# Kernel optimization log

Measured on AMD Instinct MI355X. Metric: run time of the kernel, lower is better.

## Reference

```python
import jax, jax.numpy as jnp
import numpy as np

NEG_SLOPE = 0.2

def _leaky(x):
    return jnp.where(x >= 0, x, NEG_SLOPE * x)

def _unigat(X, W, b, ae, av, pair_e, pair_v, num_v, num_e):
    # theta
    Xp = X @ W + b                                                    # [N, d]
    # v2e mean aggregation -> hyperedge features
    deg_e = jax.ops.segment_sum(jnp.ones(pair_e.shape, jnp.float32), pair_e, num_segments=num_e)
    Y = jax.ops.segment_sum(Xp[pair_v], pair_e, num_segments=num_e) / jnp.maximum(deg_e, 1.0)[:, None]  # [E, d]
    # GAT-style attention per incidence pair (edge term + node term), dropout=identity in eval
    s = _leaky((Y @ ae)[pair_e] + (Xp @ av)[pair_v])                  # [P]
    # segment softmax over edges incident to each node
    m = jax.ops.segment_max(s, pair_v, num_segments=num_v)
    ex = jnp.exp(s - m[pair_v])
    den = jax.ops.segment_sum(ex, pair_v, num_segments=num_v)
    alpha = ex / den[pair_v]                                          # [P]
    out = jax.ops.segment_sum(alpha[:, None] * Y[pair_e], pair_v, num_segments=num_v)  # [N, d]
    return jax.nn.elu(out)  # is_last=False everywhere -> ELU (use_bn=False)

def _multi_head(X, W, b, ae, av, pair_e, pair_v, num_v, num_e):
    # W:[H,din,d] b:[H,d] ae/av:[H,d]; concat heads on feature dim
    f = lambda Wh, bh, aeh, avh: _unigat(X, Wh, bh, aeh, avh, pair_e, pair_v, num_v, num_e)
    outs = jax.vmap(f)(W, b, ae, av)                                  # [H, N, d]
    return jnp.transpose(outs, (1, 0, 2)).reshape(X.shape[0], -1)     # [N, H*d]

def setup_inputs() -> dict:
    key = jax.random.key(0)
    ks = jax.random.split(key, 12)
    N, E, P = 100000, 20000, 1600000
    din, dh, H, C = 128, 64, 4, 40
    concat = 2
    inp = {
        "x0": jax.random.normal(ks[0], (N, din), jnp.float32),
        "x1": jax.random.normal(ks[1], (N, din), jnp.float32),
        "W1": jax.random.normal(ks[2], (H, din, dh), jnp.float32) * 0.05,
        "b1": jnp.zeros((H, dh), jnp.float32),
        "ae1": jax.random.normal(ks[3], (H, dh), jnp.float32) * 0.05,
        "av1": jax.random.normal(ks[4], (H, dh), jnp.float32) * 0.05,
        "W2": jax.random.normal(ks[5], (concat * dh * H, C), jnp.float32) * 0.05,
        "b2": jnp.zeros((C,), jnp.float32),
        "ae2": jax.random.normal(ks[6], (C,), jnp.float32) * 0.05,
        "av2": jax.random.normal(ks[7], (C,), jnp.float32) * 0.05,
        "pair_e": jax.random.randint(ks[8], (P,), 0, E, jnp.int32),
        "pair_v": jax.random.randint(ks[9], (P,), 0, N, jnp.int32),
        "num_v": N,
        "num_e": E,
    }
    return inp

def reference(x0, x1, W1, b1, ae1, av1, W2, b2, ae2, av2, pair_e, pair_v, num_v, num_e):
    # dropout layers are identity in eval mode
    h0 = _multi_head(x0, W1, b1, ae1, av1, pair_e, pair_v, num_v, num_e)
    h1 = _multi_head(x1, W1, b1, ae1, av1, pair_e, pair_v, num_v, num_e)
    h = jnp.concatenate([h0, h1], axis=-1)                            # [N, concat*H*dh]
    return _unigat(h, W2, b2, ae2, av2, pair_e, pair_v, num_v, num_e) # [N, C]
```

## Files before the change

### kernel.cpp

```cpp
#include <hip/hip_runtime.h>
#include <cstdint>
#include <cstddef>

static constexpr int DIN = 128;
static constexpr int DH = 64;
static constexpr int NH = 4;
static constexpr int DCAT = 512;
static constexpr int NC = 40;
static constexpr int E_CONST = 20000;
static constexpr int SH_V = 9, SUBD_V = 512;
static constexpr int SH_E = 7, SUBD_E = 128;
static constexpr int ECH = 11, NSUB_E = 10;
static constexpr int VCH = 12, NSUB_V = 25;
static constexpr int CHUNKA = 4096;

typedef unsigned short u16;
typedef __attribute__((ext_vector_type(4))) unsigned short u16x4;
typedef __attribute__((ext_vector_type(8))) unsigned short u16x8;
typedef __attribute__((ext_vector_type(8))) short bf16x8;
typedef __attribute__((ext_vector_type(4))) float f32x4;

static __device__ __forceinline__ float bf2f(u16 u) {
    union { unsigned int i; float f; } x;
    x.i = ((unsigned int)u) << 16;
    return x.f;
}
static __device__ __forceinline__ u16 f2bf(float f) {
    union { float f; unsigned int i; } x;
    x.f = f;
    unsigned int r = x.i + 0x7fffu + ((x.i >> 16) & 1u);
    return (u16)(r >> 16);
}


__global__ void k_hist2(const int* __restrict__ pv, const int* __restrict__ pe,
                        int* __restrict__ btot_v, int* __restrict__ btot_e, int P) {
    __shared__ int cv[256], ce[256];
    int tid = threadIdx.x;
    cv[tid] = 0; ce[tid] = 0;
    __syncthreads();
    int p0 = blockIdx.x * CHUNKA;
    #pragma unroll
    for (int j = 0; j < CHUNKA / 256; ++j) {
        int p = p0 + tid + j * 256;
        if (p < P) {
            atomicAdd(&cv[pv[p] >> SH_V], 1);
            atomicAdd(&ce[pe[p] >> SH_E], 1);
        }
    }
    __syncthreads();
    if (cv[tid]) atomicAdd(&btot_v[tid], cv[tid]);
    if (ce[tid]) atomicAdd(&btot_e[tid], ce[tid]);
}

__global__ void k_scan_small(int* __restrict__ a, int n) {
    __shared__ int wsum[16];
    __shared__ int carry_s;
    int tid = threadIdx.x;
    int lane = tid & 63;
    int w = tid >> 6;
    if (tid == 0) carry_s = 0;
    __syncthreads();
    for (int base = 0; base < n; base += 1024) {
        int i = base + tid;
        int v = (i < n) ? a[i] : 0;
        int x = v;
        #pragma unroll
        for (int off = 1; off < 64; off <<= 1) {
            int t = __shfl_up(x, off);
            if (lane >= off) x += t;
        }
        if (lane == 63) wsum[w] = x;
        __syncthreads();
        int woff = 0;
        for (int k = 0; k < w; ++k) woff += wsum[k];
        int carry = carry_s;
        if (i < n) a[i] = carry + woff + x - v;
        int tot = 0;
        for (int k = 0; k < 16; ++k) tot += wsum[k];
        __syncthreads();
        if (tid == 0) carry_s = carry + tot;
        __syncthreads();
    }
    if (tid == 0) a[n] = carry_s;
}

__global__ void k_scatter2way(const int* __restrict__ pv, const int* __restrict__ pe,
                              const int* __restrict__ bstart_v, const int* __restrict__ bstart_e,
                              int* __restrict__ cur_v, int* __restrict__ cur_e,
                              uint2* __restrict__ sorted_v, uint2* __restrict__ sorted_e, int P) {
    __shared__ int cv[256], ce[256], posv[256], pose[256];
    int tid = threadIdx.x;
    cv[tid] = 0; ce[tid] = 0;
    __syncthreads();
    int p0 = blockIdx.x * CHUNKA;
    int kv[CHUNKA / 256], ke[CHUNKA / 256];
    #pragma unroll
    for (int j = 0; j < CHUNKA / 256; ++j) {
        int p = p0 + tid + j * 256;
        if (p < P) {
            kv[j] = pv[p];
            ke[j] = pe[p];
            atomicAdd(&cv[kv[j] >> SH_V], 1);
            atomicAdd(&ce[ke[j] >> SH_E], 1);
        } else {
            kv[j] = -1;
            ke[j] = -1;
        }
    }
    __syncthreads();
    if (cv[tid]) posv[tid] = bstart_v[tid] + atomicAdd(&cur_v[tid], cv[tid]);
    if (ce[tid]) pose[tid] = bstart_e[tid] + atomicAdd(&cur_e[tid], ce[tid]);
    __syncthreads();
    #pragma unroll
    for (int j = 0; j < CHUNKA / 256; ++j) {
        if (kv[j] >= 0) {
            int iv = atomicAdd(&posv[kv[j] >> SH_V], 1);
            sorted_v[iv] = make_uint2((unsigned)kv[j], (unsigned)ke[j]);
            int ie = atomicAdd(&pose[ke[j] >> SH_E], 1);
            sorted_e[ie] = make_uint2((unsigned)ke[j], (unsigned)kv[j]);
        }
    }
}

template <int SUBD, int SH, int NSUB, int CSH>
__global__ __launch_bounds__(256) void k_build_ord(const uint2* __restrict__ sorted,
                                                   const int* __restrict__ bstart,
                                                   int* __restrict__ start_out,
                                                   int* __restrict__ deg_out,
                                                   int* __restrict__ csr_out, int D) {
    constexpr int NK2 = SUBD * NSUB;
    constexpr int STRIP = (NK2 + 255) / 256;
    __shared__ int cnt[NK2];
    __shared__ int wsum[4];
    int b = blockIdx.x;
    int tid = threadIdx.x;
    int base_key = b << SH;
    int s0 = bstart[b];
    int cntN = bstart[b + 1] - s0;
    for (int k = tid; k < NK2; k += 256) cnt[k] = 0;
    __syncthreads();
    for (int i = tid; i < cntN; i += 256) {
        uint2 pr = sorted[s0 + i];
        int k2 = ((int)pr.x - base_key) * NSUB + ((int)pr.y >> CSH);
        atomicAdd(&cnt[k2], 1);
    }
    __syncthreads();
    int local[STRIP];
    int sum = 0;
    int t0 = tid * STRIP;
    #pragma unroll
    for (int j = 0; j < STRIP; ++j) {
        int idx = t0 + j;
        local[j] = (idx < NK2) ? cnt[idx] : 0;
        sum += local[j];
    }
    int lane = tid & 63, w = tid >> 6;
    int x = sum;
    #pragma unroll
    for (int off = 1; off < 64; off <<= 1) {
        int t = __shfl_up(x, off);
        if (lane >= off) x += t;
    }
    if (lane == 63) wsum[w] = x;
    __syncthreads();
    int woff = 0;
    for (int k = 0; k < w; ++k) woff += wsum[k];
    int run = woff + x - sum;
    __syncthreads();
    #pragma unroll
    for (int j = 0; j < STRIP; ++j) {
        int idx = t0 + j;
        if (idx < NK2) {
            int tmp = local[j];
            cnt[idx] = run;
            run += tmp;
        }
    }
    __syncthreads();
    for (int loc = tid; loc < SUBD; loc += 256) {
        int key = base_key + loc;
        if (key < D) {
            int st = cnt[loc * NSUB];
            int en = (loc == SUBD - 1) ? cntN : cnt[(loc + 1) * NSUB];
            start_out[key] = s0 + st;
            deg_out[key] = en - st;
        }
    }
    __syncthreads();
    for (int i = tid; i < cntN; i += 256) {
        uint2 pr = sorted[s0 + i];
        int k2 = ((int)pr.x - base_key) * NSUB + ((int)pr.y >> CSH);
        int idx = atomicAdd(&cnt[k2], 1);
        csr_out[s0 + idx] = (int)pr.y;
    }
}


__global__ void k_wav(const float* __restrict__ W1, const float* __restrict__ b1,
                      const float* __restrict__ av1, float* __restrict__ wav,
                      float* __restrict__ bav) {
    int h = blockIdx.x;
    int k = threadIdx.x;
    float s = 0.f;
    for (int j = 0; j < DH; ++j) s += W1[(size_t)(h * DIN + k) * DH + j] * av1[h * DH + j];
    wav[h * DIN + k] = s;
    if (k == 0) {
        float t = 0.f;
        for (int j = 0; j < DH; ++j) t += b1[h * DH + j] * av1[h * DH + j];
        bav[h] = t;
    }
}

__global__ void k_build_wcatT(const float* __restrict__ W1, u16* __restrict__ WcatT) {
    int idx = blockIdx.x * 256 + threadIdx.x;
    if (idx >= 256 * DIN) return;
    int c = idx >> 7, k = idx & 127;
    int h = c >> 6, j = c & 63;
    WcatT[c * DIN + k] = f2bf(W1[((size_t)h * DIN + k) * DH + j]);
}

__global__ void k_build_w2T(const float* __restrict__ W2, u16* __restrict__ W2T) {
    int idx = blockIdx.x * 256 + threadIdx.x;
    if (idx >= 48 * DCAT) return;
    int c = idx >> 9, k = idx & 511;
    float v = (c < NC) ? W2[(size_t)k * NC + c] : 0.f;
    W2T[c * DCAT + k] = f2bf(v);
}

__global__ void k_conv(const float* __restrict__ X0, const float* __restrict__ X1,
                       const float* __restrict__ wav, const float* __restrict__ bav,
                       u16* __restrict__ Xbi, float* __restrict__ sv8, int N) {
    int wave = (blockIdx.x * blockDim.x + threadIdx.x) >> 6;
    int lane = threadIdx.x & 63;
    if (wave >= N) return;
    int xz = blockIdx.y;
    const float* X = xz ? X1 : X0;
    float2 a = *(const float2*)(X + (size_t)wave * DIN + lane * 2);
    unsigned int packed = (unsigned int)f2bf(a.x) | ((unsigned int)f2bf(a.y) << 16);
    *(unsigned int*)(Xbi + (size_t)wave * 256 + xz * 128 + lane * 2) = packed;
    float s[NH];
    #pragma unroll
    for (int h = 0; h < NH; ++h) {
        float2 wv = *(const float2*)(wav + h * DIN + lane * 2);
        float t = a.x * wv.x + a.y * wv.y;
        #pragma unroll
        for (int off = 32; off >= 1; off >>= 1) t += __shfl_xor(t, off);
        s[h] = t;
    }
    if (lane == 0) {
        #pragma unroll
        for (int h = 0; h < NH; ++h) sv8[(size_t)(xz * 4 + h) * N + wave] = s[h] + bav[h];
    }
}

__global__ void k_edge_mean1(const u16* __restrict__ Xbi, const int* __restrict__ start_e,
                             const int* __restrict__ deg_e, const int* __restrict__ csr_e_v,
                             u16* __restrict__ Xbar0, u16* __restrict__ Xbar1, int E) {
    int wave = (blockIdx.x * blockDim.x + threadIdx.x) >> 6;
    int lane = threadIdx.x & 63;
    if (wave >= E) return;
    int s = start_e[wave], t = s + deg_e[wave];
    int q = lane >> 4, c = lane & 15;
    float a0[8], a1[8];
    #pragma unroll
    for (int j = 0; j < 8; ++j) { a0[j] = 0.f; a1[j] = 0.f; }
    int i = s + q;
    u16x8 y0A = {0}, y1A = {0}, y0B = {0}, y1B = {0}, y0C = {0}, y1C = {0};
#define EM1_LOAD(Y0, Y1, IDX) { int v_ = csr_e_v[IDX]; \
        const u16* yp_ = Xbi + (size_t)v_ * 256 + c * 8; \
        Y0 = *(const u16x8*)yp_; Y1 = *(const u16x8*)(yp_ + 128); }
#define EM1_CONSUME(Y0, Y1) { \
        _Pragma("unroll") \
        for (int j = 0; j < 8; ++j) { a0[j] += bf2f(Y0[j]); a1[j] += bf2f(Y1[j]); } }
    if (i < t) EM1_LOAD(y0A, y1A, i);
    if (i + 4 < t) EM1_LOAD(y0B, y1B, i + 4);
    if (i + 8 < t) EM1_LOAD(y0C, y1C, i + 8);
    for (; i + 8 < t; i += 12) {
        EM1_CONSUME(y0A, y1A);
        if (i + 12 < t) EM1_LOAD(y0A, y1A, i + 12);
        EM1_CONSUME(y0B, y1B);
        if (i + 16 < t) EM1_LOAD(y0B, y1B, i + 16);
        EM1_CONSUME(y0C, y1C);
        if (i + 20 < t) EM1_LOAD(y0C, y1C, i + 20);
    }
    if (i < t) EM1_CONSUME(y0A, y1A);
    if (i + 4 < t) EM1_CONSUME(y0B, y1B);
#undef EM1_LOAD
#undef EM1_CONSUME
    #pragma unroll
    for (int j = 0; j < 8; ++j) {
        a0[j] += __shfl_xor(a0[j], 16);
        a0[j] += __shfl_xor(a0[j], 32);
        a1[j] += __shfl_xor(a1[j], 16);
        a1[j] += __shfl_xor(a1[j], 32);
    }
    int deg = t - s;
    float inv = 1.f / (float)(deg > 1 ? deg : 1);
    if (q == 0) {
        u16x8 r0, r1;
        #pragma unroll
        for (int j = 0; j < 8; ++j) { r0[j] = f2bf(a0[j] * inv); r1[j] = f2bf(a1[j] * inv); }
        *(u16x8*)(Xbar0 + (size_t)wave * DIN + c * 8) = r0;
        *(u16x8*)(Xbar1 + (size_t)wave * DIN + c * 8) = r1;
    }
}

template <int KDIM, int NTILES, int DOTMODE>
__global__ __launch_bounds__(256) void k_gemm_mfma(const u16* __restrict__ A0,
                                                   const u16* __restrict__ A1, int M,
                                                   const u16* __restrict__ Bt,
                                                   const float* __restrict__ bias,
                                                   u16* __restrict__ out0, u16* __restrict__ out1,
                                                   int ldo, int ncols,
                                                   const float* __restrict__ dvec,
                                                   float* __restrict__ dout) {
    constexpr int LDB = KDIM + 8;
    __shared__ u16 Bs[NTILES * 16 * LDB];
    const u16* A = blockIdx.z ? A1 : A0;
    u16* out = blockIdx.z ? out1 : out0;
    int tid = threadIdx.x;
    int colbase = blockIdx.y * NTILES * 16;
    const u16* Btblk = Bt + (size_t)colbase * KDIM;
    for (int idx = tid * 4; idx < NTILES * 16 * KDIM; idx += 256 * 4) {
        int c = idx / KDIM, k = idx % KDIM;
        *(u16x4*)&Bs[c * LDB + k] = *(const u16x4*)(Btblk + c * KDIM + k);
    }
    __syncthreads();
    int w = tid >> 6, lane = tid & 63;
    int r0 = blockIdx.x * 64 + w * 16;
    int arow = r0 + (lane & 15);
    bool avalid = arow < M;
    const u16* ap = A + (size_t)arow * KDIM + (lane >> 4) * 8;
    f32x4 acc[NTILES];
    #pragma unroll
    for (int nt = 0; nt < NTILES; ++nt) acc[nt] = (f32x4){0.f, 0.f, 0.f, 0.f};
    #pragma unroll
    for (int k0 = 0; k0 < KDIM; k0 += 32) {
        bf16x8 a = (bf16x8)(short)0;
        if (avalid) a = *(const bf16x8*)(ap + k0);
        #pragma unroll
        for (int nt = 0; nt < NTILES; ++nt) {
            bf16x8 b = *(const bf16x8*)&Bs[(nt * 16 + (lane & 15)) * LDB + k0 + (lane >> 4) * 8];
            acc[nt] = __builtin_amdgcn_mfma_f32_16x16x32_bf16(a, b, acc[nt], 0, 0, 0);
        }
    }
    #pragma unroll
    for (int j = 0; j < 4; ++j) {
        int row = r0 + (lane >> 4) * 4 + j;
        float pA = 0.f, pB = 0.f;
        #pragma unroll
        for (int nt = 0; nt < NTILES; ++nt) {
            int col = colbase + nt * 16 + (lane & 15);
            bool cok = col < ncols;
            float val = cok ? acc[nt][j] + bias[col] : 0.f;
            if (DOTMODE == 1) {
                float dv = dvec[col];
                if (nt < NTILES / 2) pA += val * dv; else pB += val * dv;
            } else if (DOTMODE == 2) {
                pA += cok ? val * dvec[col] : 0.f;
            }
            if (row < M && cok) out[(size_t)row * ldo + col] = f2bf(val);
        }
        if (DOTMODE) {
            pA += __shfl_xor(pA, 1);
            pA += __shfl_xor(pA, 2);
            pA += __shfl_xor(pA, 4);
            pA += __shfl_xor(pA, 8);
            if (DOTMODE == 1) {
                pB += __shfl_xor(pB, 1);
                pB += __shfl_xor(pB, 2);
                pB += __shfl_xor(pB, 4);
                pB += __shfl_xor(pB, 8);
            }
            if ((lane & 15) == 0 && row < M) {
                if (DOTMODE == 1) {
                    int hbase = blockIdx.y * 2;
                    int z = blockIdx.z;
                    dout[(size_t)(z * 4 + hbase) * M + row] = pA;
                    dout[(size_t)(z * 4 + hbase + 1) * M + row] = pB;
                } else {
                    dout[row] = pA;
                }
            }
        }
    }
}

__global__ void k_node_pass1(const u16* __restrict__ Ycat, const float* __restrict__ se8,
                             const float* __restrict__ sv8, const int* __restrict__ start_v,
                             const int* __restrict__ deg_v, const int* __restrict__ csr_v_e,
                             u16* __restrict__ hbuf, int N, int E) {
    int bid = blockIdx.x;
    int s = bid & 7;
    int warp = threadIdx.x >> 6;
    int lane = threadIdx.x & 63;
    int g = lane >> 3, c = lane & 7;
    int node = (bid >> 3) * 32 + warp * 8 + g;
    if (node >= N) return;
    int p0 = start_v[node];
    int p1 = p0 + deg_v[node];
    float sv = sv8[(size_t)s * N + node];
    const float* seS = se8 + (size_t)s * E;
    const u16* ybase = Ycat + s * 64 + c * 8;
    float den = 0.f;
    float acc[8];
    #pragma unroll
    for (int j = 0; j < 8; ++j) acc[j] = 0.f;
    for (int i = p0; i < p1; ++i) {
        int e = csr_v_e[i];
        float x = seS[e] + sv;
        x = fmaxf(x, 0.2f * x);
        float ex = __expf(x);
        den += ex;
        u16x8 y = *(const u16x8*)(ybase + (size_t)e * 512);
        #pragma unroll
        for (int j = 0; j < 8; ++j) acc[j] += ex * bf2f(y[j]);
    }
    float inv = (p1 > p0) ? 1.f / den : 0.f;
    u16x8 r;
    #pragma unroll
    for (int j = 0; j < 8; ++j) {
        float o = acc[j] * inv;
        o = o > 0.f ? o : __expf(o) - 1.f;
        r[j] = f2bf(o);
    }
    *(u16x8*)(hbuf + (size_t)node * DCAT + s * 64 + c * 8) = r;
}


__global__ void k_edge_mean2(const u16* __restrict__ Xp2b, const int* __restrict__ start_e,
                             const int* __restrict__ deg_ea, const int* __restrict__ csr_e_v,
                             u16* __restrict__ Y2b, const float* __restrict__ ae2,
                             float* __restrict__ se2, int E) {
    int wave = (blockIdx.x * blockDim.x + threadIdx.x) >> 6;
    int lane = threadIdx.x & 63;
    if (wave >= E) return;
    int s = start_e[wave], t = s + deg_ea[wave];
    int g = lane >> 4, c = lane & 15;
    bool act = c < 10;
    float acc[4];
    #pragma unroll
    for (int j = 0; j < 4; ++j) acc[j] = 0.f;
    for (int i = s + g; i < t; i += 4) {
        int v = csr_e_v[i];
        if (act) {
            u16x4 y = *(const u16x4*)(Xp2b + (size_t)v * NC + c * 4);
            acc[0] += bf2f(y.x);
            acc[1] += bf2f(y.y);
            acc[2] += bf2f(y.z);
            acc[3] += bf2f(y.w);
        }
    }
    #pragma unroll
    for (int j = 0; j < 4; ++j) {
        acc[j] += __shfl_xor(acc[j], 16);
        acc[j] += __shfl_xor(acc[j], 32);
    }
    int deg = t - s;
    float inv = 1.f / (float)(deg > 1 ? deg : 1);
    float p = 0.f;
    if (act) {
        float4 ae = *(const float4*)(ae2 + c * 4);
        float y0 = acc[0] * inv, y1 = acc[1] * inv, y2 = acc[2] * inv, y3 = acc[3] * inv;
        p = y0 * ae.x + y1 * ae.y + y2 * ae.z + y3 * ae.w;
        if (g == 0) {
            u16x4 r = {f2bf(y0), f2bf(y1), f2bf(y2), f2bf(y3)};
            *(u16x4*)(Y2b + (size_t)wave * NC + c * 4) = r;
        }
    }
    #pragma unroll
    for (int off = 8; off >= 1; off >>= 1) p += __shfl_xor(p, off);
    if (lane == 0) se2[wave] = p;
}

__global__ void k_node_pass2(const u16* __restrict__ Y2b, const float* __restrict__ se2,
                             const float* __restrict__ sv2, const int* __restrict__ start_v,
                             const int* __restrict__ deg_va, const int* __restrict__ csr_v_e,
                             float* __restrict__ out, int N) {
    int wave = (blockIdx.x * blockDim.x + threadIdx.x) >> 6;
    int lane = threadIdx.x & 63;
    if (wave >= N) return;
    int s = start_v[wave], t = s + deg_va[wave];
    int g = lane >> 4, c = lane & 15;
    bool act = c < 10;
    float* orow = out + (size_t)wave * NC;
    if (t == s) {
        if (g == 0 && act) *(float4*)(orow + c * 4) = make_float4(0.f, 0.f, 0.f, 0.f);
        return;
    }
    float svv = sv2[wave];
    float den = 0.f;
    float acc[4];
    #pragma unroll
    for (int j = 0; j < 4; ++j) acc[j] = 0.f;
    for (int i = s + g; i < t; i += 4) {
        int e = csr_v_e[i];
        float x = se2[e] + svv;
        x = fmaxf(x, 0.2f * x);
        float ex = __expf(x);
        den += ex;
        if (act) {
            u16x4 y = *(const u16x4*)(Y2b + (size_t)e * NC + c * 4);
            acc[0] += ex * bf2f(y.x);
            acc[1] += ex * bf2f(y.y);
            acc[2] += ex * bf2f(y.z);
            acc[3] += ex * bf2f(y.w);
        }
    }
    den += __shfl_xor(den, 16);
    den += __shfl_xor(den, 32);
    #pragma unroll
    for (int j = 0; j < 4; ++j) {
        acc[j] += __shfl_xor(acc[j], 16);
        acc[j] += __shfl_xor(acc[j], 32);
    }
    if (g == 0 && act) {
        float inv = 1.f / den;
        float4 o;
        float* op = &o.x;
        #pragma unroll
        for (int j = 0; j < 4; ++j) {
            float v = acc[j] * inv;
            op[j] = v > 0.f ? v : __expf(v) - 1.f;
        }
        *(float4*)(orow + c * 4) = o;
    }
}

extern "C" void kernel_launch(void* const* d_in, const int* in_sizes, int n_in,
                              void* d_out, int out_size, void* d_ws, size_t ws_size,
                              hipStream_t stream) {
    const float* x0 = (const float*)d_in[0];
    const float* x1 = (const float*)d_in[1];
    const float* W1 = (const float*)d_in[2];
    const float* b1 = (const float*)d_in[3];
    const float* ae1 = (const float*)d_in[4];
    const float* av1 = (const float*)d_in[5];
    const float* W2 = (const float*)d_in[6];
    const float* b2 = (const float*)d_in[7];
    const float* ae2 = (const float*)d_in[8];
    const float* av2 = (const float*)d_in[9];
    const int* pe = (const int*)d_in[10];
    const int* pv = (const int*)d_in[11];

    const int N = in_sizes[0] / DIN;
    const int P = in_sizes[10];
    const int E = E_CONST;
    const int NBKT_V = (N + SUBD_V - 1) / SUBD_V;
    const int NBKT_E = (E + SUBD_E - 1) / SUBD_E;

    char* base = (char*)d_ws;
    auto alloc = [&](size_t bytes) -> void* {
        void* p = (void*)base;
        base += (bytes + 255) & ~(size_t)255;
        return p;
    };
    u16* Xbi = (u16*)alloc((size_t)N * 256 * 2);
    u16* hbuf = (u16*)alloc((size_t)N * DCAT * 2);
    u16* Xbar0 = (u16*)alloc((size_t)E * DIN * 2);
    u16* Xbar1 = (u16*)alloc((size_t)E * DIN * 2);
    u16* Ycat = (u16*)alloc((size_t)E * 512 * 2);
    u16* Xp2b = (u16*)alloc((size_t)N * NC * 2);
    u16* Y2b = (u16*)alloc((size_t)E * NC * 2);
    float* se8 = (float*)alloc((size_t)8 * E * 4);
    float* se2 = (float*)alloc((size_t)E * 4);
    float* sv8 = (float*)alloc((size_t)8 * N * 4);
    float* sv2 = (float*)alloc((size_t)N * 4);
    float* wav = (float*)alloc((size_t)NH * DIN * 4);
    float* bav = (float*)alloc((size_t)NH * 4);
    u16* WcatT = (u16*)alloc((size_t)256 * DIN * 2);
    u16* W2T = (u16*)alloc((size_t)48 * DCAT * 2);
    uint2* sorted_v = (uint2*)alloc((size_t)P * 8);
    uint2* sorted_e = (uint2*)alloc((size_t)P * 8);
    int* start_v = (int*)alloc((size_t)N * 4);
    int* deg_v = (int*)alloc((size_t)N * 4);
    int* start_e = (int*)alloc((size_t)E * 4);
    int* deg_e = (int*)alloc((size_t)E * 4);
    int* csr_v_e = (int*)alloc((size_t)P * 4);
    int* csr_e_v = (int*)alloc((size_t)P * 4);
    char* zstart = base;
    int* bstart_v = (int*)alloc((size_t)(NBKT_V + 1) * 4);
    int* bstart_e = (int*)alloc((size_t)(NBKT_E + 1) * 4);
    int* cur_v = (int*)alloc((size_t)256 * 4);
    int* cur_e = (int*)alloc((size_t)256 * 4);
    size_t zbytes = (size_t)(base - zstart);

    if ((size_t)(base - (char*)d_ws) > ws_size) return;

    hipMemsetAsync(zstart, 0, zbytes, stream);

    dim3 b256(256);
    int nA = (P + CHUNKA - 1) / CHUNKA;
    k_hist2<<<nA, b256, 0, stream>>>(pv, pe, bstart_v, bstart_e, P);
    k_scan_small<<<1, 1024, 0, stream>>>(bstart_v, NBKT_V);
    k_scan_small<<<1, 1024, 0, stream>>>(bstart_e, NBKT_E);
    k_scatter2way<<<nA, b256, 0, stream>>>(pv, pe, bstart_v, bstart_e, cur_v, cur_e,
                                           sorted_v, sorted_e, P);
    k_build_ord<SUBD_V, SH_V, NSUB_E, ECH><<<NBKT_V, b256, 0, stream>>>(sorted_v, bstart_v,
                                                                        start_v, deg_v,
                                                                        csr_v_e, N);
    k_build_ord<SUBD_E, SH_E, NSUB_V, VCH><<<NBKT_E, b256, 0, stream>>>(sorted_e, bstart_e,
                                                                        start_e, deg_e,
                                                                        csr_e_v, E);

    k_wav<<<NH, DIN, 0, stream>>>(W1, b1, av1, wav, bav);
    k_build_wcatT<<<(256 * DIN + 255) / 256, b256, 0, stream>>>(W1, WcatT);
    k_build_w2T<<<(48 * DCAT + 255) / 256, b256, 0, stream>>>(W2, W2T);

    int gN4 = (N + 3) / 4;
    int gE4 = (E + 3) / 4;
    dim3 gconv(gN4, 2);
    k_conv<<<gconv, b256, 0, stream>>>(x0, x1, wav, bav, Xbi, sv8, N);

    k_edge_mean1<<<gE4, b256, 0, stream>>>(Xbi, start_e, deg_e, csr_e_v, Xbar0, Xbar1, E);
    dim3 g1((E + 63) / 64, 2, 2);
    k_gemm_mfma<DIN, 8, 1><<<g1, b256, 0, stream>>>(Xbar0, Xbar1, E, WcatT, b1,
                                                    Ycat, Ycat + 256, 512, 256, ae1, se8);
    int gnp1 = ((N + 31) / 32) * 8;
    k_node_pass1<<<gnp1, b256, 0, stream>>>(Ycat, se8, sv8, start_v, deg_v, csr_v_e,
                                            hbuf, N, E);

    dim3 g2((N + 63) / 64, 1, 1);
    k_gemm_mfma<DCAT, 3, 2><<<g2, b256, 0, stream>>>(hbuf, hbuf, N, W2T, b2, Xp2b, Xp2b,
                                                     NC, NC, av2, sv2);
    k_edge_mean2<<<gE4, b256, 0, stream>>>(Xp2b, start_e, deg_e, csr_e_v, Y2b, ae2, se2, E);
    k_node_pass2<<<gN4, b256, 0, stream>>>(Y2b, se2, sv2, start_v, deg_v, csr_v_e,
                                           (float*)d_out, N);
}
```

Measured before the change: 642.5 us.

## Merge setup kernels, software-pipeline node pass 1, remap layer-2 segment kernels

Combines the two scan launches into one two-block kernel and the three weight-prep kernels into one launch, which removes launch overhead. In node pass 1 the per-edge loop is double-buffered so the index, score and Y-row loads for the next two edges are issued before the current one is consumed, hiding gather latency. Layer-2 edge-mean and node-pass kernels now map 8 segments per wave with 8 lanes each, using 16-byte loads, instead of one segment per wave with 4-way strided partial sums and shuffles. This trades intra-segment parallelism for more segments in flight and fewer wasted lanes, but lanes with uneven degrees may diverge more.

```diff
diff --git a/kernel.cpp b/kernel.cpp
--- a/kernel.cpp
+++ b/kernel.cpp
@@ -53,7 +53,7 @@
     if (ce[tid]) atomicAdd(&btot_e[tid], ce[tid]);
 }
 
-__global__ void k_scan_small(int* __restrict__ a, int n) {
+static __device__ void scan_body(int* a, int n) {
     __shared__ int wsum[16];
     __shared__ int carry_s;
     int tid = threadIdx.x;
@@ -83,6 +83,11 @@
         __syncthreads();
     }
     if (tid == 0) a[n] = carry_s;
+}
+
+__global__ void k_scan_both(int* __restrict__ a, int na, int* __restrict__ b, int nb) {
+    if (blockIdx.x == 0) scan_body(a, na);
+    else scan_body(b, nb);
 }
 
 __global__ void k_scatter2way(const int* __restrict__ pv, const int* __restrict__ pe,
@@ -196,36 +201,36 @@
     }
 }
 
-
-__global__ void k_wav(const float* __restrict__ W1, const float* __restrict__ b1,
-                      const float* __restrict__ av1, float* __restrict__ wav,
-                      float* __restrict__ bav) {
-    int h = blockIdx.x;
-    int k = threadIdx.x;
-    float s = 0.f;
-    for (int j = 0; j < DH; ++j) s += W1[(size_t)(h * DIN + k) * DH + j] * av1[h * DH + j];
-    wav[h * DIN + k] = s;
-    if (k == 0) {
-        float t = 0.f;
-        for (int j = 0; j < DH; ++j) t += b1[h * DH + j] * av1[h * DH + j];
-        bav[h] = t;
-    }
-}
-
-__global__ void k_build_wcatT(const float* __restrict__ W1, u16* __restrict__ WcatT) {
-    int idx = blockIdx.x * 256 + threadIdx.x;
-    if (idx >= 256 * DIN) return;
-    int c = idx >> 7, k = idx & 127;
-    int h = c >> 6, j = c & 63;
-    WcatT[c * DIN + k] = f2bf(W1[((size_t)h * DIN + k) * DH + j]);
-}
-
-__global__ void k_build_w2T(const float* __restrict__ W2, u16* __restrict__ W2T) {
-    int idx = blockIdx.x * 256 + threadIdx.x;
-    if (idx >= 48 * DCAT) return;
-    int c = idx >> 9, k = idx & 511;
-    float v = (c < NC) ? W2[(size_t)k * NC + c] : 0.f;
-    W2T[c * DCAT + k] = f2bf(v);
+__global__ void k_prep(const float* __restrict__ W1, const float* __restrict__ b1,
+                       const float* __restrict__ av1, const float* __restrict__ W2,
+                       float* __restrict__ wav, float* __restrict__ bav,
+                       u16* __restrict__ WcatT, u16* __restrict__ W2T) {
+    int bid = blockIdx.x;
+    int tid = threadIdx.x;
+    if (bid < 4) {
+        int h = bid;
+        if (tid < DIN) {
+            float s = 0.f;
+            for (int j = 0; j < DH; ++j)
+                s += W1[(size_t)(h * DIN + tid) * DH + j] * av1[h * DH + j];
+            wav[h * DIN + tid] = s;
+        }
+        if (tid == 0) {
+            float t = 0.f;
+            for (int j = 0; j < DH; ++j) t += b1[h * DH + j] * av1[h * DH + j];
+            bav[h] = t;
+        }
+    } else if (bid < 4 + 128) {
+        int idx = (bid - 4) * 256 + tid;
+        int c = idx >> 7, k = idx & 127;
+        int h = c >> 6, j = c & 63;
+        WcatT[c * DIN + k] = f2bf(W1[((size_t)h * DIN + k) * DH + j]);
+    } else {
+        int idx = (bid - 132) * 256 + tid;
+        int c = idx >> 9, k = idx & 511;
+        float v = (c < NC) ? W2[(size_t)k * NC + c] : 0.f;
+        W2T[c * DCAT + k] = f2bf(v);
+    }
 }
 
 __global__ void k_conv(const float* __restrict__ X0, const float* __restrict__ X1,
@@ -407,16 +412,27 @@
     float acc[8];
     #pragma unroll
     for (int j = 0; j < 8; ++j) acc[j] = 0.f;
-    for (int i = p0; i < p1; ++i) {
-        int e = csr_v_e[i];
-        float x = seS[e] + sv;
-        x = fmaxf(x, 0.2f * x);
-        float ex = __expf(x);
-        den += ex;
-        u16x8 y = *(const u16x8*)(ybase + (size_t)e * 512);
-        #pragma unroll
-        for (int j = 0; j < 8; ++j) acc[j] += ex * bf2f(y[j]);
-    }
+    float sA = 0.f, sB = 0.f;
+    u16x8 yA = {0}, yB = {0};
+#define NP1_LOAD(S, Y, IDX) { int e_ = csr_v_e[IDX]; S = seS[e_]; \
+        Y = *(const u16x8*)(ybase + (size_t)e_ * 512); }
+#define NP1_CONSUME(S, Y) { \
+        float x_ = S + sv; x_ = fmaxf(x_, 0.2f * x_); float ex_ = __expf(x_); \
+        den += ex_; \
+        _Pragma("unroll") \
+        for (int j = 0; j < 8; ++j) acc[j] += ex_ * bf2f(Y[j]); }
+    int i = p0;
+    if (i < p1) NP1_LOAD(sA, yA, i);
+    if (i + 1 < p1) NP1_LOAD(sB, yB, i + 1);
+    for (; i + 1 < p1; i += 2) {
+        NP1_CONSUME(sA, yA);
+        if (i + 2 < p1) NP1_LOAD(sA, yA, i + 2);
+        NP1_CONSUME(sB, yB);
+        if (i + 3 < p1) NP1_LOAD(sB, yB, i + 3);
+    }
+    if (i < p1) NP1_CONSUME(sA, yA);
+#undef NP1_LOAD
+#undef NP1_CONSUME
     float inv = (p1 > p0) ? 1.f / den : 0.f;
     u16x8 r;
     #pragma unroll
@@ -433,98 +449,91 @@
                              const int* __restrict__ deg_ea, const int* __restrict__ csr_e_v,
                              u16* __restrict__ Y2b, const float* __restrict__ ae2,
                              float* __restrict__ se2, int E) {
-    int wave = (blockIdx.x * blockDim.x + threadIdx.x) >> 6;
+    int warp = threadIdx.x >> 6;
     int lane = threadIdx.x & 63;
-    if (wave >= E) return;
-    int s = start_e[wave], t = s + deg_ea[wave];
-    int g = lane >> 4, c = lane & 15;
-    bool act = c < 10;
-    float acc[4];
-    #pragma unroll
-    for (int j = 0; j < 4; ++j) acc[j] = 0.f;
-    for (int i = s + g; i < t; i += 4) {
-        int v = csr_e_v[i];
-        if (act) {
-            u16x4 y = *(const u16x4*)(Xp2b + (size_t)v * NC + c * 4);
-            acc[0] += bf2f(y.x);
-            acc[1] += bf2f(y.y);
-            acc[2] += bf2f(y.z);
-            acc[3] += bf2f(y.w);
-        }
-    }
-    #pragma unroll
-    for (int j = 0; j < 4; ++j) {
-        acc[j] += __shfl_xor(acc[j], 16);
-        acc[j] += __shfl_xor(acc[j], 32);
-    }
-    int deg = t - s;
+    int g = lane >> 3, c = lane & 7;
+    int edge = blockIdx.x * 32 + warp * 8 + g;
+    if (edge >= E) return;
+    int p0 = start_e[edge], p1 = p0 + deg_ea[edge];
+    bool act = c < 5;
+    const u16* xbase = Xp2b + c * 8;
+    float acc[8];
+    #pragma unroll
+    for (int j = 0; j < 8; ++j) acc[j] = 0.f;
+    if (act) {
+        for (int i = p0; i < p1; ++i) {
+            int v = csr_e_v[i];
+            u16x8 y = *(const u16x8*)(xbase + (size_t)v * NC);
+            #pragma unroll
+            for (int j = 0; j < 8; ++j) acc[j] += bf2f(y[j]);
+        }
+    }
+    int deg = p1 - p0;
     float inv = 1.f / (float)(deg > 1 ? deg : 1);
     float p = 0.f;
     if (act) {
-        float4 ae = *(const float4*)(ae2 + c * 4);
-        float y0 = acc[0] * inv, y1 = acc[1] * inv, y2 = acc[2] * inv, y3 = acc[3] * inv;
-        p = y0 * ae.x + y1 * ae.y + y2 * ae.z + y3 * ae.w;
-        if (g == 0) {
-            u16x4 r = {f2bf(y0), f2bf(y1), f2bf(y2), f2bf(y3)};
-            *(u16x4*)(Y2b + (size_t)wave * NC + c * 4) = r;
-        }
-    }
-    #pragma unroll
-    for (int off = 8; off >= 1; off >>= 1) p += __shfl_xor(p, off);
-    if (lane == 0) se2[wave] = p;
+        u16x8 r;
+        #pragma unroll
+        for (int j = 0; j < 8; ++j) {
+            float y = acc[j] * inv;
+            p += y * ae2[c * 8 + j];
+            r[j] = f2bf(y);
+        }
+        *(u16x8*)(Y2b + (size_t)edge * NC + c * 8) = r;
+    }
+    p += __shfl_xor(p, 1);
+    p += __shfl_xor(p, 2);
+    p += __shfl_xor(p, 4);
+    if (c == 0) se2[edge] = p;
 }
 
 __global__ void k_node_pass2(const u16* __restrict__ Y2b, const float* __restrict__ se2,
                              const float* __restrict__ sv2, const int* __restrict__ start_v,
                              const int* __restrict__ deg_va, const int* __restrict__ csr_v_e,
                              float* __restrict__ out, int N) {
-    int wave = (blockIdx.x * blockDim.x + threadIdx.x) >> 6;
+    int warp = threadIdx.x >> 6;
     int lane = threadIdx.x & 63;
-    if (wave >= N) return;
-    int s = start_v[wave], t = s + deg_va[wave];
-    int g = lane >> 4, c = lane & 15;
-    bool act = c < 10;
-    float* orow = out + (size_t)wave * NC;
-    if (t == s) {
-        if (g == 0 && act) *(float4*)(orow + c * 4) = make_float4(0.f, 0.f, 0.f, 0.f);
+    int g = lane >> 3, c = lane & 7;
+    int node = blockIdx.x * 32 + warp * 8 + g;
+    if (node >= N) return;
+    int p0 = start_v[node], p1 = p0 + deg_va[node];
+    bool act = c < 5;
+    float* orow = out + (size_t)node * NC;
+    if (p1 == p0) {
+        if (act) {
+            *(float4*)(orow + c * 8) = make_float4(0.f, 0.f, 0.f, 0.f);
+            *(float4*)(orow + c * 8 + 4) = make_float4(0.f, 0.f, 0.f, 0.f);
+        }
         return;
     }
-    float svv = sv2[wave];
+    float svv = sv2[node];
+    const u16* ybase = Y2b + c * 8;
     float den = 0.f;
-    float acc[4];
-    #pragma unroll
-    for (int j = 0; j < 4; ++j) acc[j] = 0.f;
-    for (int i = s + g; i < t; i += 4) {
+    float acc[8];
+    #pragma unroll
+    for (int j = 0; j < 8; ++j) acc[j] = 0.f;
+    for (int i = p0; i < p1; ++i) {
         int e = csr_v_e[i];
         float x = se2[e] + svv;
         x = fmaxf(x, 0.2f * x);
         float ex = __expf(x);
         den += ex;
         if (act) {
-            u16x4 y = *(const u16x4*)(Y2b + (size_t)e * NC + c * 4);
-            acc[0] += ex * bf2f(y.x);
-            acc[1] += ex * bf2f(y.y);
-            acc[2] += ex * bf2f(y.z);
-            acc[3] += ex * bf2f(y.w);
-        }
-    }
-    den += __shfl_xor(den, 16);
-    den += __shfl_xor(den, 32);
-    #pragma unroll
-    for (int j = 0; j < 4; ++j) {
-        acc[j] += __shfl_xor(acc[j], 16);
-        acc[j] += __shfl_xor(acc[j], 32);
-    }
-    if (g == 0 && act) {
+            u16x8 y = *(const u16x8*)(ybase + (size_t)e * NC);
+            #pragma unroll
+            for (int j = 0; j < 8; ++j) acc[j] += ex * bf2f(y[j]);
+        }
+    }
+    if (act) {
         float inv = 1.f / den;
-        float4 o;
-        float* op = &o.x;
-        #pragma unroll
-        for (int j = 0; j < 4; ++j) {
+        float o[8];
+        #pragma unroll
+        for (int j = 0; j < 8; ++j) {
             float v = acc[j] * inv;
-            op[j] = v > 0.f ? v : __expf(v) - 1.f;
-        }
-        *(float4*)(orow + c * 4) = o;
+            o[j] = v > 0.f ? v : __expf(v) - 1.f;
+        }
+        *(float4*)(orow + c * 8) = make_float4(o[0], o[1], o[2], o[3]);
+        *(float4*)(orow + c * 8 + 4) = make_float4(o[4], o[5], o[6], o[7]);
     }
 }
 
@@ -593,8 +602,7 @@
     dim3 b256(256);
     int nA = (P + CHUNKA - 1) / CHUNKA;
     k_hist2<<<nA, b256, 0, stream>>>(pv, pe, bstart_v, bstart_e, P);
-    k_scan_small<<<1, 1024, 0, stream>>>(bstart_v, NBKT_V);
-    k_scan_small<<<1, 1024, 0, stream>>>(bstart_e, NBKT_E);
+    k_scan_both<<<2, 1024, 0, stream>>>(bstart_v, NBKT_V, bstart_e, NBKT_E);
     k_scatter2way<<<nA, b256, 0, stream>>>(pv, pe, bstart_v, bstart_e, cur_v, cur_e,
                                            sorted_v, sorted_e, P);
     k_build_ord<SUBD_V, SH_V, NSUB_E, ECH><<<NBKT_V, b256, 0, stream>>>(sorted_v, bstart_v,
@@ -604,9 +612,7 @@
                                                                         start_e, deg_e,
                                                                         csr_e_v, E);
 
-    k_wav<<<NH, DIN, 0, stream>>>(W1, b1, av1, wav, bav);
-    k_build_wcatT<<<(256 * DIN + 255) / 256, b256, 0, stream>>>(W1, WcatT);
-    k_build_w2T<<<(48 * DCAT + 255) / 256, b256, 0, stream>>>(W2, W2T);
+    k_prep<<<228, b256, 0, stream>>>(W1, b1, av1, W2, wav, bav, WcatT, W2T);
 
     int gN4 = (N + 3) / 4;
     int gE4 = (E + 3) / 4;
@@ -624,7 +630,9 @@
     dim3 g2((N + 63) / 64, 1, 1);
     k_gemm_mfma<DCAT, 3, 2><<<g2, b256, 0, stream>>>(hbuf, hbuf, N, W2T, b2, Xp2b, Xp2b,
                                                      NC, NC, av2, sv2);
-    k_edge_mean2<<<gE4, b256, 0, stream>>>(Xp2b, start_e, deg_e, csr_e_v, Y2b, ae2, se2, E);
-    k_node_pass2<<<gN4, b256, 0, stream>>>(Y2b, se2, sv2, start_v, deg_v, csr_v_e,
-                                           (float*)d_out, N);
-}
+    int gseg = (E + 31) / 32;
+    k_edge_mean2<<<gseg, b256, 0, stream>>>(Xp2b, start_e, deg_e, csr_e_v, Y2b, ae2, se2, E);
+    int gnp2 = (N + 31) / 32;
+    k_node_pass2<<<gnp2, b256, 0, stream>>>(Y2b, se2, sv2, start_v, deg_v, csr_v_e,
+                                            (float*)d_out, N);
+}
```

New measurement: 600.5 us. 1.07x faster.
